# Kernel tuning notes

Measured on AMD Instinct MI355X. Metric: run time of the kernel, lower is better.

## Reference

```python
import jax, jax.numpy as jnp
import numpy as np

N, E, G = 20000, 240000, 64
F, H1, PE = 768, 128, 32
D = H1 + PE          # 160, GATv2 per-head dim
HEADS = 5
HC = HEADS * D       # 800
H2, OUT = 128, 16
NEG_SLOPE = 0.2


def setup_inputs() -> dict:
    key = jax.random.key(0)
    ks = jax.random.split(key, 24)
    s = 0.02
    inp = {
        'x': jax.random.normal(ks[0], (N, F), jnp.float32),
        'pe_enc': jax.random.normal(ks[1], (N, PE), jnp.float32),
        'edge_index': jax.random.randint(ks[2], (2, E), 0, N),
        'batch': jnp.sort(jax.random.randint(ks[3], (N,), 0, G)),
        'flat_weight': jax.random.uniform(ks[4], (N, 1), jnp.float32),
        'num_graphs': G,
        # params
        'W_pre': jax.random.normal(ks[5], (F, H1)) * s,
        'b_pre': jnp.zeros((H1,)),
        'W_l': jax.random.normal(ks[6], (D, HC)) * s,
        'b_l': jnp.zeros((HC,)),
        'W_r': jax.random.normal(ks[7], (D, HC)) * s,
        'b_r': jnp.zeros((HC,)),
        'att': jax.random.normal(ks[8], (HEADS, D)) * s,
        'gat_bias': jnp.zeros((HC,)),
        'W_gcn': jax.random.normal(ks[9], (HC, HC)) * s,
        'b_gcn': jnp.zeros((HC,)),
        'W_fc': jax.random.normal(ks[10], (2 * HC, H2)) * s,
        'b_fc': jnp.zeros((H2,)),
        'W_out': jax.random.normal(ks[11], (H2, OUT)) * s,
        'b_out': jnp.zeros((OUT,)),
    }
    return inp


def _forward(x, pe_enc, flat_weight, W_pre, b_pre, W_l, b_l, W_r, b_r, att,
             gat_bias, W_gcn, b_gcn, W_fc, b_fc, W_out, b_out,
             edge_index, batch, num_graphs):
    n = x.shape[0]
    # pre-FC + PE concat -> [N, D]
    h = jnp.concatenate([jax.nn.relu(x @ W_pre + b_pre), pe_enc], axis=1)
    # add self loops (PyG default for GATv2Conv and GCNConv)
    ar = jnp.arange(n)
    src = jnp.concatenate([edge_index[0], ar])
    dst = jnp.concatenate([edge_index[1], ar])
    # ---- GATv2Conv ----
    x_l = (h @ W_l + b_l).reshape(n, HEADS, D)
    x_r = (h @ W_r + b_r).reshape(n, HEADS, D)
    m = x_l[src] + x_r[dst]                                # [Et, H, D]
    score = (jnp.where(m > 0, m, NEG_SLOPE * m) * att).sum(-1)  # [Et, H]
    smax = jax.ops.segment_max(score, dst, num_segments=n)[dst]
    ex = jnp.exp(score - smax)
    den = jax.ops.segment_sum(ex, dst, num_segments=n)[dst]
    alpha = ex / den                                       # softmax per target
    agg = jax.ops.segment_sum(x_l[src] * alpha[..., None], dst, num_segments=n)
    g1 = jax.nn.relu(agg.reshape(n, HC) + gat_bias)
    # ---- GCNConv with symmetric normalization ----
    deg = jax.ops.segment_sum(jnp.ones_like(dst, dtype=g1.dtype), dst, num_segments=n)
    dinv = jnp.where(deg > 0, deg ** -0.5, 0.0)
    norm = dinv[src] * dinv[dst]
    hg = g1 @ W_gcn
    g2 = jax.nn.relu(jax.ops.segment_sum(hg[src] * norm[:, None], dst, num_segments=n) + b_gcn)
    # ---- weighted mean pool + max pool ----
    ps = jax.ops.segment_sum(g2 * flat_weight, batch, num_segments=num_graphs)
    ws = jnp.clip(jax.ops.segment_sum(flat_weight, batch, num_segments=num_graphs), 1e-6, None)
    pooled_mean = ps / ws
    mx = jax.ops.segment_max(g2, batch, num_segments=num_graphs)
    mx = jnp.where(jnp.isneginf(mx), 0.0, mx)  # empty graphs; g2 >= 0 after relu
    gfeat = jnp.concatenate([pooled_mean, mx], axis=1)     # [G, 2*HC]
    out = jax.nn.relu(gfeat @ W_fc + b_fc)                 # dropout is identity in eval
    return jax.nn.relu(out @ W_out + b_out)


def reference(x, pe_enc, edge_index, batch, flat_weight, num_graphs,
              W_pre, b_pre, W_l, b_l, W_r, b_r, att, gat_bias,
              W_gcn, b_gcn, W_fc, b_fc, W_out, b_out):
    return _forward(x, pe_enc, flat_weight, W_pre, b_pre, W_l, b_l, W_r, b_r,
                    att, gat_bias, W_gcn, b_gcn, W_fc, b_fc, W_out, b_out,
                    edge_index, batch, num_graphs)
```

## Files before the change

### kernel.cpp

```cpp
#include <hip/hip_runtime.h>
#include <hip/hip_bf16.h>

#define Nn     20000
#define Ee     240000
#define Gg     64
#define Ff     768
#define H1c    128
#define PEc    32
#define Dd     160
#define HEADSc 5
#define HCc    800
#define H2c    128
#define OUTc   16
#define ETot   (Ee + Nn)
#define NEG_SLOPE_F 0.2f

typedef short bf16x8 __attribute__((ext_vector_type(8)));
typedef float f32x4 __attribute__((ext_vector_type(4)));
typedef unsigned int u32;

__device__ __forceinline__ unsigned short bf_hi_rn(float v) {
    unsigned int u = __float_as_uint(v);
    return (unsigned short)((u + 0x7FFFu + ((u >> 16) & 1u)) >> 16);
}
__device__ __forceinline__ void bsplit(float v, unsigned short& h, unsigned short& l) {
    unsigned short hh = bf_hi_rn(v);
    float hf = __uint_as_float(((unsigned int)hh) << 16);
    l = bf_hi_rn(v - hf);
    h = hh;
}

__device__ __forceinline__ void gl_lds16(const unsigned short* g, unsigned short* l) {
    __builtin_amdgcn_global_load_lds(
        (const __attribute__((address_space(1))) u32*)g,
        (__attribute__((address_space(3))) u32*)l, 16, 0, 0);
}

__global__ void asplit_kernel(const float* __restrict__ A, unsigned short* __restrict__ Ah,
                              unsigned short* __restrict__ Al, int total4) {
    int i = blockIdx.x * 256 + threadIdx.x;
    if (i < total4) {
        float4 v = ((const float4*)A)[i];
        ushort4 h4, l4;
        bsplit(v.x, h4.x, l4.x);
        bsplit(v.y, h4.y, l4.y);
        bsplit(v.z, h4.z, l4.z);
        bsplit(v.w, h4.w, l4.w);
        ((ushort4*)Ah)[i] = h4;
        ((ushort4*)Al)[i] = l4;
    }
}

__global__ void wsplit_kernel(const float* __restrict__ W, unsigned short* __restrict__ Wh,
                              unsigned short* __restrict__ Wl, int K, int N) {
    int i = blockIdx.x * 256 + threadIdx.x;
    if (i < K * N) {
        int k = i / N, n = i % N;
        unsigned short h, l;
        bsplit(W[i], h, l);
        Wh[(size_t)n * K + k] = h;
        Wl[(size_t)n * K + k] = l;
    }
}

#define KCHUNK 32

template<int ROWS>
__device__ __forceinline__ void stage_tile(const unsigned short* __restrict__ gsrc, int ld,
                                           int row0, int maxRow, int k0,
                                           unsigned short* lbuf, int wave, int lane) {
    #pragma unroll
    for (int p = 0; p < ROWS / 64; ++p) {
        int rb = wave * 16 + p * 64;
        int r = rb + (lane >> 2);
        int gr = min(row0 + r, maxRow);
        const unsigned short* g = gsrc + (size_t)gr * ld + k0 + (lane & 3) * 8;
        gl_lds16(g, lbuf + rb * 32);
    }
}

template<int BM, int BN, int OUT_MODE>
__global__ __launch_bounds__(256)
void gemm3_kernel(const unsigned short* __restrict__ Ah, const unsigned short* __restrict__ Al,
                  const unsigned short* __restrict__ Bh, const unsigned short* __restrict__ Bl,
                  const float* __restrict__ bias, float* __restrict__ C,
                  unsigned short* __restrict__ Ch, unsigned short* __restrict__ Cl,
                  int M, int N, int K, int lda, int ldc, int relu) {
    constexpr int TM = BM / 32;
    constexpr int TN = BN / 32;
    __shared__ __attribute__((aligned(16))) unsigned short As_h[BM * 32];
    __shared__ __attribute__((aligned(16))) unsigned short As_l[BM * 32];
    __shared__ __attribute__((aligned(16))) unsigned short Bs_h[BN * 32];
    __shared__ __attribute__((aligned(16))) unsigned short Bs_l[BN * 32];

    int tid = threadIdx.x;
    int m0 = blockIdx.x * BM, n0 = blockIdx.y * BN;
    int wave = tid >> 6, lane = tid & 63;
    int wm = (wave >> 1) * (16 * TM);
    int wn = (wave & 1) * (16 * TN);
    int fr = lane & 15;
    int fq = (lane >> 4) * 8;

    f32x4 acc[TM][TN] = {};

    for (int k0 = 0; k0 < K; k0 += KCHUNK) {
        stage_tile<BM>(Ah, lda, m0, M - 1, k0, As_h, wave, lane);
        stage_tile<BM>(Al, lda, m0, M - 1, k0, As_l, wave, lane);
        stage_tile<BN>(Bh, K,   n0, N - 1, k0, Bs_h, wave, lane);
        stage_tile<BN>(Bl, K,   n0, N - 1, k0, Bs_l, wave, lane);
        __syncthreads();

        bf16x8 a_h[TM], a_l[TM], b_h[TN], b_l[TN];
        #pragma unroll
        for (int i = 0; i < TM; ++i) {
            a_h[i] = *(const bf16x8*)&As_h[(wm + i * 16 + fr) * 32 + fq];
            a_l[i] = *(const bf16x8*)&As_l[(wm + i * 16 + fr) * 32 + fq];
        }
        #pragma unroll
        for (int j = 0; j < TN; ++j) {
            b_h[j] = *(const bf16x8*)&Bs_h[(wn + j * 16 + fr) * 32 + fq];
            b_l[j] = *(const bf16x8*)&Bs_l[(wn + j * 16 + fr) * 32 + fq];
        }
        #pragma unroll
        for (int j = 0; j < TN; ++j) {
            #pragma unroll
            for (int i = 0; i < TM; ++i) {
                acc[i][j] = __builtin_amdgcn_mfma_f32_16x16x32_bf16(a_h[i], b_h[j], acc[i][j], 0, 0, 0);
                acc[i][j] = __builtin_amdgcn_mfma_f32_16x16x32_bf16(a_h[i], b_l[j], acc[i][j], 0, 0, 0);
                acc[i][j] = __builtin_amdgcn_mfma_f32_16x16x32_bf16(a_l[i], b_h[j], acc[i][j], 0, 0, 0);
            }
        }
        __syncthreads();
    }

    int cr = (lane >> 4) * 4, cc = lane & 15;
    #pragma unroll
    for (int i = 0; i < TM; ++i) {
        #pragma unroll
        for (int j = 0; j < TN; ++j) {
            int c = n0 + wn + j * 16 + cc;
            if (c >= N) continue;
            float bv = bias ? bias[c] : 0.f;
            #pragma unroll
            for (int reg = 0; reg < 4; ++reg) {
                int r = m0 + wm + i * 16 + cr + reg;
                if (r >= M) continue;
                float v = acc[i][j][reg] + bv;
                if (relu) v = fmaxf(v, 0.f);
                if (OUT_MODE == 0) {
                    C[(size_t)r * ldc + c] = v;
                } else {
                    unsigned short hh, ll;
                    bsplit(v, hh, ll);
                    Ch[(size_t)r * ldc + c] = hh;
                    Cl[(size_t)r * ldc + c] = ll;
                }
            }
        }
    }
}

__global__ void pe_copy_kernel(const float* __restrict__ pe, unsigned short* __restrict__ hh,
                               unsigned short* __restrict__ hl) {
    int i = blockIdx.x * 256 + threadIdx.x;
    if (i < Nn * PEc) {
        int n = i / PEc, j = i % PEc;
        unsigned short h, l;
        bsplit(pe[i], h, l);
        hh[(size_t)n * Dd + H1c + j] = h;
        hl[(size_t)n * Dd + H1c + j] = l;
    }
}

__global__ void count_kernel(const int* __restrict__ eidx, int* __restrict__ cnt) {
    int e = blockIdx.x * 256 + threadIdx.x;
    if (e < Ee) atomicAdd(&cnt[eidx[Ee + e]], 1);
}

#define NBLK 79
__global__ void scan1_kernel(const int* __restrict__ cnt, int* __restrict__ off,
                             int* __restrict__ bsum) {
    __shared__ int sh[256];
    int t = threadIdx.x, i = blockIdx.x * 256 + t;
    int v = (i < Nn) ? (cnt[i] + 1) : 0;
    sh[t] = v;
    __syncthreads();
    for (int ofs = 1; ofs < 256; ofs <<= 1) {
        int add = (t >= ofs) ? sh[t - ofs] : 0;
        __syncthreads();
        sh[t] += add;
        __syncthreads();
    }
    if (i < Nn) off[i] = sh[t] - v;
    if (t == 255) bsum[blockIdx.x] = sh[255];
}
__global__ void scan2_kernel(int* __restrict__ bsum) {
    if (threadIdx.x == 0) {
        int acc = 0;
        for (int b = 0; b < NBLK; ++b) { int v = bsum[b]; bsum[b] = acc; acc += v; }
    }
}
__global__ void scan3_kernel(const int* __restrict__ cnt, int* __restrict__ off,
                             int* __restrict__ nxt, float* __restrict__ dinv,
                             const int* __restrict__ bsum) {
    int i = blockIdx.x * 256 + threadIdx.x;
    if (i < Nn) {
        int o = off[i] + bsum[blockIdx.x];
        off[i] = o;
        nxt[i] = o;
        dinv[i] = rsqrtf((float)(cnt[i] + 1));
    }
    if (i == 0) off[Nn] = ETot;
}

__global__ void scatter_kernel(const int* __restrict__ eidx, int* __restrict__ nxt,
                               int* __restrict__ elist, int* __restrict__ edst) {
    int e = blockIdx.x * 256 + threadIdx.x;
    if (e < ETot) {
        int s, d;
        if (e < Ee) { s = eidx[e]; d = eidx[Ee + e]; }
        else        { s = e - Ee; d = s; }
        int slot = atomicAdd(&nxt[d], 1);
        elist[slot] = s;
        edst[slot] = d;
    }
}

#define FCH 8
__global__ __launch_bounds__(256)
void fused_gat_kernel(const float* __restrict__ xl, const float* __restrict__ xr,
                      const float* __restrict__ att, const int* __restrict__ elist,
                      const int* __restrict__ off, const float* __restrict__ gat_bias,
                      unsigned short* __restrict__ g1h, unsigned short* __restrict__ g1l) {
    int d = blockIdx.x;
    int t = threadIdx.x;
    __shared__ float sh_red[FCH][200];
    __shared__ float sh_sc[FCH][HEADSc];
    __shared__ float sh_w[FCH][HEADSc];
    __shared__ float sh_scale[HEADSc], sh_m[HEADSc], sh_den[HEADSc];
    __shared__ int sh_src[FCH];
    int e0 = off[d], e1 = off[d + 1];
    int cnt = e1 - e0;
    bool act = t < 200;
    int hd = act ? (t / 40) : 0;
    float4 vr = {0.f, 0.f, 0.f, 0.f}, va = {0.f, 0.f, 0.f, 0.f};
    if (act) {
        vr = ((const float4*)(xr + (size_t)d * HCc))[t];
        va = ((const float4*)att)[t];
    }
    if (t < HEADSc) { sh_m[t] = -1e30f; sh_den[t] = 0.f; }
    float4 acc = {0.f, 0.f, 0.f, 0.f};

    for (int base = 0; base < cnt; base += FCH) {
        int nc = min(FCH, cnt - base);
        if (t < FCH) sh_src[t] = elist[e0 + base + min(t, nc - 1)];
        __syncthreads();
        float4 vl[FCH];
        if (act) {
            #pragma unroll
            for (int e = 0; e < FCH; ++e)
                vl[e] = ((const float4*)(xl + (size_t)sh_src[e] * HCc))[t];
            #pragma unroll
            for (int e = 0; e < FCH; ++e) {
                float p = 0.f, m, lm;
                m = vl[e].x + vr.x; lm = fmaxf(m, 0.2f * m); p = fmaf(lm, va.x, p);
                m = vl[e].y + vr.y; lm = fmaxf(m, 0.2f * m); p = fmaf(lm, va.y, p);
                m = vl[e].z + vr.z; lm = fmaxf(m, 0.2f * m); p = fmaf(lm, va.z, p);
                m = vl[e].w + vr.w; lm = fmaxf(m, 0.2f * m); p = fmaf(lm, va.w, p);
                sh_red[e][t] = p;
            }
        }
        __syncthreads();
        if (t < 40) {
            int e = t & 7, h = t >> 3;
            float s = 0.f;
            const float* pr = &sh_red[e][h * 40];
            #pragma unroll
            for (int k = 0; k < 40; ++k) s += pr[k];
            sh_sc[e][h] = (e < nc) ? s : -1e30f;
        }
        if (t < HEADSc) {
            float mo = sh_m[t];
            float mn = mo;
            #pragma unroll
            for (int e = 0; e < FCH; ++e) mn = fmaxf(mn, sh_sc[e][t]);
            float sc = __expf(mo - mn);
            float den = sh_den[t] * sc;
            #pragma unroll
            for (int e = 0; e < FCH; ++e) {
                float w = __expf(sh_sc[e][t] - mn);
                sh_w[e][t] = w;
                den += w;
            }
            sh_den[t] = den;
            sh_m[t] = mn;
            sh_scale[t] = sc;
        }
        __syncthreads();
        if (act) {
            float sc = sh_scale[hd];
            acc.x *= sc; acc.y *= sc; acc.z *= sc; acc.w *= sc;
            #pragma unroll
            for (int e = 0; e < FCH; ++e) {
                float w = sh_w[e][hd];
                acc.x = fmaf(w, vl[e].x, acc.x);
                acc.y = fmaf(w, vl[e].y, acc.y);
                acc.z = fmaf(w, vl[e].z, acc.z);
                acc.w = fmaf(w, vl[e].w, acc.w);
            }
        }
    }
    if (act) {
        float inv = 1.f / sh_den[hd];
        float4 bv = ((const float4*)gat_bias)[t];
        ushort4 oh, ol;
        float v;
        v = fmaxf(fmaf(acc.x, inv, bv.x), 0.f); bsplit(v, oh.x, ol.x);
        v = fmaxf(fmaf(acc.y, inv, bv.y), 0.f); bsplit(v, oh.y, ol.y);
        v = fmaxf(fmaf(acc.z, inv, bv.z), 0.f); bsplit(v, oh.z, ol.z);
        v = fmaxf(fmaf(acc.w, inv, bv.w), 0.f); bsplit(v, oh.w, ol.w);
        *(ushort4*)(g1h + (size_t)d * HCc + 4 * t) = oh;
        *(ushort4*)(g1l + (size_t)d * HCc + 4 * t) = ol;
    }
}

__global__ __launch_bounds__(256)
void gcn_kernel(const float* __restrict__ hg, const float* __restrict__ dinv,
                const int* __restrict__ elist, const int* __restrict__ off,
                const float* __restrict__ b_gcn, float* __restrict__ g2) {
    int d = blockIdx.x;
    int t = threadIdx.x;
    __shared__ int src_s[64];
    __shared__ float w_s[64];
    int e0 = off[d], e1 = off[d + 1];
    int cnt = e1 - e0;
    float di = dinv[d];
    float4 acc = {0.f, 0.f, 0.f, 0.f};
    for (int base = 0; base < cnt; base += 64) {
        int nc = min(64, cnt - base);
        if (t < nc) {
            int s = elist[e0 + base + t];
            src_s[t] = s;
            w_s[t] = dinv[s];
        }
        __syncthreads();
        if (t < 200) {
            for (int el = 0; el < nc; ++el) {
                const float4* p = (const float4*)(hg + (size_t)src_s[el] * HCc);
                float w = w_s[el];
                float4 v = p[t];
                acc.x = fmaf(w, v.x, acc.x);
                acc.y = fmaf(w, v.y, acc.y);
                acc.z = fmaf(w, v.z, acc.z);
                acc.w = fmaf(w, v.w, acc.w);
            }
        }
        __syncthreads();
    }
    if (t < 200) {
        float4 bv = ((const float4*)b_gcn)[t];
        float4 o;
        o.x = fmaxf(acc.x * di + bv.x, 0.f);
        o.y = fmaxf(acc.y * di + bv.y, 0.f);
        o.z = fmaxf(acc.z * di + bv.z, 0.f);
        o.w = fmaxf(acc.w * di + bv.w, 0.f);
        *(float4*)(g2 + (size_t)d * HCc + 4 * t) = o;
    }
}

__global__ void bounds_kernel(const int* __restrict__ batch, int* __restrict__ starts) {
    int g = threadIdx.x;
    if (g <= Gg) {
        if (g == Gg) { starts[Gg] = Nn; return; }
        int lo = 0, hi = Nn;
        while (lo < hi) {
            int mid = (lo + hi) >> 1;
            if (batch[mid] < g) lo = mid + 1; else hi = mid;
        }
        starts[g] = lo;
    }
}

#define PSL 4
__global__ __launch_bounds__(256)
void pool1_kernel(const float* __restrict__ g2, const float* __restrict__ fw,
                  const int* __restrict__ starts, float* __restrict__ pw,
                  float* __restrict__ pmean, float* __restrict__ pmax) {
    int g = blockIdx.x, s = blockIdx.y, t = threadIdx.x;
    int n0 = starts[g], n1 = starts[g + 1];
    int len = n1 - n0;
    int q0 = n0 + (int)(((long long)len * s) / PSL);
    int q1 = n0 + (int)(((long long)len * (s + 1)) / PSL);
    __shared__ float red[256];
    float wsum = 0.f;
    for (int n = q0 + t; n < q1; n += 256) wsum += fw[n];
    red[t] = wsum;
    __syncthreads();
    for (int ofs = 128; ofs > 0; ofs >>= 1) {
        if (t < ofs) red[t] += red[t + ofs];
        __syncthreads();
    }
    if (t == 0) pw[g * PSL + s] = red[0];
    if (t < 200) {
        float4 sum = {0.f, 0.f, 0.f, 0.f};
        float4 mx = {0.f, 0.f, 0.f, 0.f};
        for (int n = q0; n < q1; ++n) {
            float w = fw[n];
            float4 v = ((const float4*)(g2 + (size_t)n * HCc))[t];
            sum.x = fmaf(w, v.x, sum.x); sum.y = fmaf(w, v.y, sum.y);
            sum.z = fmaf(w, v.z, sum.z); sum.w = fmaf(w, v.w, sum.w);
            mx.x = fmaxf(mx.x, v.x); mx.y = fmaxf(mx.y, v.y);
            mx.z = fmaxf(mx.z, v.z); mx.w = fmaxf(mx.w, v.w);
        }
        size_t o = ((size_t)g * PSL + s) * HCc + 4 * t;
        *(float4*)(pmean + o) = sum;
        *(float4*)(pmax + o) = mx;
    }
}
__global__ __launch_bounds__(256)
void pool2_kernel(const float* __restrict__ pw, const float* __restrict__ pmean,
                  const float* __restrict__ pmax, float* __restrict__ gfeat) {
    int g = blockIdx.x, t = threadIdx.x;
    if (t >= 200) return;
    float wsg = 0.f;
    #pragma unroll
    for (int s = 0; s < PSL; ++s) wsg += pw[g * PSL + s];
    wsg = fmaxf(wsg, 1e-6f);
    float inv = 1.f / wsg;
    float4 sum = {0.f, 0.f, 0.f, 0.f};
    float4 mx = {0.f, 0.f, 0.f, 0.f};
    #pragma unroll
    for (int s = 0; s < PSL; ++s) {
        size_t o = ((size_t)g * PSL + s) * HCc + 4 * t;
        float4 a = *(const float4*)(pmean + o);
        float4 b = *(const float4*)(pmax + o);
        sum.x += a.x; sum.y += a.y; sum.z += a.z; sum.w += a.w;
        mx.x = fmaxf(mx.x, b.x); mx.y = fmaxf(mx.y, b.y);
        mx.z = fmaxf(mx.z, b.z); mx.w = fmaxf(mx.w, b.w);
    }
    float* gm = gfeat + (size_t)g * (2 * HCc);
    sum.x *= inv; sum.y *= inv; sum.z *= inv; sum.w *= inv;
    *(float4*)(gm + 4 * t) = sum;
    *(float4*)(gm + HCc + 4 * t) = mx;
}

__global__ __launch_bounds__(128)
void head_kernel(const float* __restrict__ gfeat, const float* __restrict__ W_fc,
                 const float* __restrict__ b_fc, const float* __restrict__ W_out,
                 const float* __restrict__ b_out, float* __restrict__ out) {
    int g = blockIdx.x;
    int t = threadIdx.x;
    __shared__ float gf[2 * HCc];
    __shared__ float fc1[H2c];
    for (int i = t; i < 2 * HCc; i += 128) gf[i] = gfeat[(size_t)g * (2 * HCc) + i];
    __syncthreads();
    float a0 = 0.f, a1 = 0.f, a2 = 0.f, a3 = 0.f;
    for (int k = 0; k < 2 * HCc; k += 4) {
        a0 = fmaf(gf[k],     W_fc[(size_t)k * H2c + t], a0);
        a1 = fmaf(gf[k + 1], W_fc[(size_t)(k + 1) * H2c + t], a1);
        a2 = fmaf(gf[k + 2], W_fc[(size_t)(k + 2) * H2c + t], a2);
        a3 = fmaf(gf[k + 3], W_fc[(size_t)(k + 3) * H2c + t], a3);
    }
    fc1[t] = fmaxf(b_fc[t] + ((a0 + a1) + (a2 + a3)), 0.f);
    __syncthreads();
    if (t < OUTc) {
        float o = b_out[t];
        #pragma unroll 8
        for (int k = 0; k < H2c; ++k) o += fc1[k] * W_out[k * OUTc + t];
        out[g * OUTc + t] = fmaxf(o, 0.f);
    }
}

extern "C" void kernel_launch(void* const* d_in, const int* in_sizes, int n_in,
                              void* d_out, int out_size, void* d_ws, size_t ws_size,
                              hipStream_t stream) {
    (void)in_sizes; (void)n_in; (void)out_size; (void)ws_size;
    const float* x        = (const float*)d_in[0];
    const float* pe       = (const float*)d_in[1];
    const int*   eidx     = (const int*)d_in[2];
    const int*   batch    = (const int*)d_in[3];
    const float* fw       = (const float*)d_in[4];
    const float* W_pre    = (const float*)d_in[6];
    const float* b_pre    = (const float*)d_in[7];
    const float* W_l      = (const float*)d_in[8];
    const float* b_l      = (const float*)d_in[9];
    const float* W_r      = (const float*)d_in[10];
    const float* b_r      = (const float*)d_in[11];
    const float* att      = (const float*)d_in[12];
    const float* gat_bias = (const float*)d_in[13];
    const float* W_gcn    = (const float*)d_in[14];
    const float* b_gcn    = (const float*)d_in[15];
    const float* W_fc     = (const float*)d_in[16];
    const float* b_fc     = (const float*)d_in[17];
    const float* W_out    = (const float*)d_in[18];
    const float* b_out    = (const float*)d_in[19];
    float* out = (float*)d_out;

    char* p = (char*)d_ws;
    auto alloc = [&](size_t bytes) {
        char* r = p;
        p += (bytes + 255) & ~(size_t)255;
        return r;
    };
    unsigned short* hh = (unsigned short*)alloc((size_t)Nn * Dd * 2 * 2);
    unsigned short* hl = hh + (size_t)Nn * Dd;
    float* bufA = (float*)alloc((size_t)Nn * HCc * 4);
    float* bufB = (float*)alloc((size_t)Nn * HCc * 4);
    float* bufC = (float*)alloc((size_t)Nn * HCc * 4);
    int*   cnt    = (int*)alloc((size_t)Nn * 4);
    int*   off    = (int*)alloc((size_t)(Nn + 1) * 4);
    int*   nxt    = (int*)alloc((size_t)Nn * 4);
    float* dinv   = (float*)alloc((size_t)Nn * 4);
    int*   elist  = (int*)alloc((size_t)ETot * 4);
    int*   edst   = (int*)alloc((size_t)ETot * 4);
    int*   starts = (int*)alloc((size_t)(Gg + 1) * 4);
    float* gfeat  = (float*)alloc((size_t)Gg * 2 * HCc * 4);
    int*   bsum   = (int*)alloc((size_t)NBLK * 4);
    float* pw     = (float*)alloc((size_t)Gg * PSL * 4);
    float* pmean  = (float*)alloc((size_t)Gg * PSL * HCc * 4);
    float* pmax   = (float*)alloc((size_t)Gg * PSL * HCc * 4);
    unsigned short* WpreTh = (unsigned short*)alloc((size_t)Ff * H1c * 2 * 2);
    unsigned short* WpreTl = WpreTh + (size_t)Ff * H1c;
    unsigned short* WlTh   = (unsigned short*)alloc((size_t)Dd * HCc * 2 * 2);
    unsigned short* WlTl   = WlTh + (size_t)Dd * HCc;
    unsigned short* WrTh   = (unsigned short*)alloc((size_t)Dd * HCc * 2 * 2);
    unsigned short* WrTl   = WrTh + (size_t)Dd * HCc;
    unsigned short* WgTh   = (unsigned short*)alloc((size_t)HCc * HCc * 2 * 2);
    unsigned short* WgTl   = WgTh + (size_t)HCc * HCc;

    unsigned short* xh  = (unsigned short*)bufC;
    unsigned short* xlo = xh + (size_t)Nn * Ff;
    unsigned short* g1h = (unsigned short*)bufC;
    unsigned short* g1l = g1h + (size_t)Nn * HCc;

    hipMemsetAsync(cnt, 0, (size_t)Nn * 4, stream);
    count_kernel<<<(Ee + 255) / 256, 256, 0, stream>>>(eidx, cnt);
    scan1_kernel<<<NBLK, 256, 0, stream>>>(cnt, off, bsum);
    scan2_kernel<<<1, 64, 0, stream>>>(bsum);
    scan3_kernel<<<NBLK, 256, 0, stream>>>(cnt, off, nxt, dinv, bsum);
    scatter_kernel<<<(ETot + 255) / 256, 256, 0, stream>>>(eidx, nxt, elist, edst);

    asplit_kernel<<<(Nn * Ff / 4 + 255) / 256, 256, 0, stream>>>(x, xh, xlo, Nn * Ff / 4);
    wsplit_kernel<<<(Ff * H1c + 255) / 256, 256, 0, stream>>>(W_pre, WpreTh, WpreTl, Ff, H1c);
    wsplit_kernel<<<(Dd * HCc + 255) / 256, 256, 0, stream>>>(W_l, WlTh, WlTl, Dd, HCc);
    wsplit_kernel<<<(Dd * HCc + 255) / 256, 256, 0, stream>>>(W_r, WrTh, WrTl, Dd, HCc);
    wsplit_kernel<<<(HCc * HCc + 255) / 256, 256, 0, stream>>>(W_gcn, WgTh, WgTl, HCc, HCc);

    {
        dim3 grid((Nn + 63) / 64, (H1c + 63) / 64);
        gemm3_kernel<64, 64, 1><<<grid, 256, 0, stream>>>(
            xh, xlo, WpreTh, WpreTl, b_pre, nullptr, hh, hl,
            Nn, H1c, Ff, Ff, Dd, 1);
    }
    pe_copy_kernel<<<(Nn * PEc + 255) / 256, 256, 0, stream>>>(pe, hh, hl);

    {
        dim3 grid((Nn + 127) / 128, (HCc + 127) / 128);
        gemm3_kernel<128, 128, 0><<<grid, 256, 0, stream>>>(
            hh, hl, WlTh, WlTl, b_l, bufA, nullptr, nullptr,
            Nn, HCc, Dd, Dd, HCc, 0);
        gemm3_kernel<128, 128, 0><<<grid, 256, 0, stream>>>(
            hh, hl, WrTh, WrTl, b_r, bufB, nullptr, nullptr,
            Nn, HCc, Dd, Dd, HCc, 0);
    }

    fused_gat_kernel<<<Nn, 256, 0, stream>>>(bufA, bufB, att, elist, off,
                                             gat_bias, g1h, g1l);

    {
        dim3 grid((Nn + 127) / 128, (HCc + 127) / 128);
        gemm3_kernel<128, 128, 0><<<grid, 256, 0, stream>>>(
            g1h, g1l, WgTh, WgTl, nullptr, bufA, nullptr, nullptr,
            Nn, HCc, HCc, HCc, HCc, 0);
    }
    gcn_kernel<<<Nn, 256, 0, stream>>>(bufA, dinv, elist, off, b_gcn, bufB);

    bounds_kernel<<<1, 128, 0, stream>>>(batch, starts);
    {
        dim3 pg(Gg, PSL);
        pool1_kernel<<<pg, 256, 0, stream>>>(bufB, fw, starts, pw, pmean, pmax);
    }
    pool2_kernel<<<Gg, 256, 0, stream>>>(pw, pmean, pmax, gfeat);
    head_kernel<<<Gg, 128, 0, stream>>>(gfeat, W_fc, b_fc, W_out, b_out, out);
}
```

Measured before the change: 805.0 us.

## Merge left/right GAT projections into one GEMM and batch edge gathers

```diff
diff --git a/kernel.cpp b/kernel.cpp
--- a/kernel.cpp
+++ b/kernel.cpp
@@ -83,7 +83,8 @@
 __global__ __launch_bounds__(256)
 void gemm3_kernel(const unsigned short* __restrict__ Ah, const unsigned short* __restrict__ Al,
                   const unsigned short* __restrict__ Bh, const unsigned short* __restrict__ Bl,
-                  const float* __restrict__ bias, float* __restrict__ C,
+                  const float* __restrict__ bias, const float* __restrict__ bias2,
+                  float* __restrict__ C, float* __restrict__ C2,
                   unsigned short* __restrict__ Ch, unsigned short* __restrict__ Cl,
                   int M, int N, int K, int lda, int ldc, int relu) {
     constexpr int TM = BM / 32;
@@ -140,7 +141,9 @@
         for (int j = 0; j < TN; ++j) {
             int c = n0 + wn + j * 16 + cc;
             if (c >= N) continue;
-            float bv = bias ? bias[c] : 0.f;
+            float bv;
+            if (OUT_MODE == 2) bv = (c < HCc) ? bias[c] : bias2[c - HCc];
+            else bv = bias ? bias[c] : 0.f;
             #pragma unroll
             for (int reg = 0; reg < 4; ++reg) {
                 int r = m0 + wm + i * 16 + cr + reg;
@@ -149,6 +152,9 @@
                 if (relu) v = fmaxf(v, 0.f);
                 if (OUT_MODE == 0) {
                     C[(size_t)r * ldc + c] = v;
+                } else if (OUT_MODE == 2) {
+                    if (c < HCc) C[(size_t)r * HCc + c] = v;
+                    else         C2[(size_t)r * HCc + (c - HCc)] = v;
                 } else {
                     unsigned short hh, ll;
                     bsplit(v, hh, ll);
@@ -214,7 +220,7 @@
 }
 
 __global__ void scatter_kernel(const int* __restrict__ eidx, int* __restrict__ nxt,
-                               int* __restrict__ elist, int* __restrict__ edst) {
+                               int* __restrict__ elist) {
     int e = blockIdx.x * 256 + threadIdx.x;
     if (e < ETot) {
         int s, d;
@@ -222,11 +228,10 @@
         else        { s = e - Ee; d = s; }
         int slot = atomicAdd(&nxt[d], 1);
         elist[slot] = s;
-        edst[slot] = d;
-    }
-}
-
-#define FCH 8
+    }
+}
+
+#define FCH 16
 __global__ __launch_bounds__(256)
 void fused_gat_kernel(const float* __restrict__ xl, const float* __restrict__ xr,
                       const float* __restrict__ att, const int* __restrict__ elist,
@@ -273,11 +278,13 @@
         __syncthreads();
         if (t < 40) {
             int e = t & 7, h = t >> 3;
-            float s = 0.f;
-            const float* pr = &sh_red[e][h * 40];
-            #pragma unroll
-            for (int k = 0; k < 40; ++k) s += pr[k];
-            sh_sc[e][h] = (e < nc) ? s : -1e30f;
+            float s0 = 0.f, s1 = 0.f;
+            const float* p0 = &sh_red[e][h * 40];
+            const float* p1 = &sh_red[e + 8][h * 40];
+            #pragma unroll
+            for (int k = 0; k < 40; ++k) { s0 += p0[k]; s1 += p1[k]; }
+            sh_sc[e][h]     = (e < nc)     ? s0 : -1e30f;
+            sh_sc[e + 8][h] = (e + 8 < nc) ? s1 : -1e30f;
         }
         if (t < HEADSc) {
             float mo = sh_m[t];
@@ -324,40 +331,45 @@
     }
 }
 
+#define GCH 16
 __global__ __launch_bounds__(256)
 void gcn_kernel(const float* __restrict__ hg, const float* __restrict__ dinv,
                 const int* __restrict__ elist, const int* __restrict__ off,
                 const float* __restrict__ b_gcn, float* __restrict__ g2) {
     int d = blockIdx.x;
     int t = threadIdx.x;
-    __shared__ int src_s[64];
-    __shared__ float w_s[64];
+    __shared__ int src_s[GCH];
+    __shared__ float w_s[GCH];
     int e0 = off[d], e1 = off[d + 1];
     int cnt = e1 - e0;
     float di = dinv[d];
+    bool act = t < 200;
     float4 acc = {0.f, 0.f, 0.f, 0.f};
-    for (int base = 0; base < cnt; base += 64) {
-        int nc = min(64, cnt - base);
-        if (t < nc) {
-            int s = elist[e0 + base + t];
+    for (int base = 0; base < cnt; base += GCH) {
+        int nc = min(GCH, cnt - base);
+        if (t < GCH) {
+            int s = elist[e0 + base + min(t, nc - 1)];
             src_s[t] = s;
-            w_s[t] = dinv[s];
-        }
-        __syncthreads();
-        if (t < 200) {
-            for (int el = 0; el < nc; ++el) {
-                const float4* p = (const float4*)(hg + (size_t)src_s[el] * HCc);
-                float w = w_s[el];
-                float4 v = p[t];
-                acc.x = fmaf(w, v.x, acc.x);
-                acc.y = fmaf(w, v.y, acc.y);
-                acc.z = fmaf(w, v.z, acc.z);
-                acc.w = fmaf(w, v.w, acc.w);
+            w_s[t] = (t < nc) ? dinv[s] : 0.f;
+        }
+        __syncthreads();
+        if (act) {
+            float4 vl[GCH];
+            #pragma unroll
+            for (int e = 0; e < GCH; ++e)
+                vl[e] = ((const float4*)(hg + (size_t)src_s[e] * HCc))[t];
+            #pragma unroll
+            for (int e = 0; e < GCH; ++e) {
+                float w = w_s[e];
+                acc.x = fmaf(w, vl[e].x, acc.x);
+                acc.y = fmaf(w, vl[e].y, acc.y);
+                acc.z = fmaf(w, vl[e].z, acc.z);
+                acc.w = fmaf(w, vl[e].w, acc.w);
             }
         }
         __syncthreads();
     }
-    if (t < 200) {
+    if (act) {
         float4 bv = ((const float4*)b_gcn)[t];
         float4 o;
         o.x = fmaxf(acc.x * di + bv.x, 0.f);
@@ -512,7 +524,6 @@
     int*   nxt    = (int*)alloc((size_t)Nn * 4);
     float* dinv   = (float*)alloc((size_t)Nn * 4);
     int*   elist  = (int*)alloc((size_t)ETot * 4);
-    int*   edst   = (int*)alloc((size_t)ETot * 4);
     int*   starts = (int*)alloc((size_t)(Gg + 1) * 4);
     float* gfeat  = (float*)alloc((size_t)Gg * 2 * HCc * 4);
     int*   bsum   = (int*)alloc((size_t)NBLK * 4);
@@ -521,10 +532,8 @@
     float* pmax   = (float*)alloc((size_t)Gg * PSL * HCc * 4);
     unsigned short* WpreTh = (unsigned short*)alloc((size_t)Ff * H1c * 2 * 2);
     unsigned short* WpreTl = WpreTh + (size_t)Ff * H1c;
-    unsigned short* WlTh   = (unsigned short*)alloc((size_t)Dd * HCc * 2 * 2);
-    unsigned short* WlTl   = WlTh + (size_t)Dd * HCc;
-    unsigned short* WrTh   = (unsigned short*)alloc((size_t)Dd * HCc * 2 * 2);
-    unsigned short* WrTl   = WrTh + (size_t)Dd * HCc;
+    unsigned short* WlrTh  = (unsigned short*)alloc((size_t)Dd * 2 * HCc * 2 * 2);
+    unsigned short* WlrTl  = WlrTh + (size_t)Dd * 2 * HCc;
     unsigned short* WgTh   = (unsigned short*)alloc((size_t)HCc * HCc * 2 * 2);
     unsigned short* WgTl   = WgTh + (size_t)HCc * HCc;
 
@@ -538,39 +547,37 @@
     scan1_kernel<<<NBLK, 256, 0, stream>>>(cnt, off, bsum);
     scan2_kernel<<<1, 64, 0, stream>>>(bsum);
     scan3_kernel<<<NBLK, 256, 0, stream>>>(cnt, off, nxt, dinv, bsum);
-    scatter_kernel<<<(ETot + 255) / 256, 256, 0, stream>>>(eidx, nxt, elist, edst);
+    scatter_kernel<<<(ETot + 255) / 256, 256, 0, stream>>>(eidx, nxt, elist);
 
     asplit_kernel<<<(Nn * Ff / 4 + 255) / 256, 256, 0, stream>>>(x, xh, xlo, Nn * Ff / 4);
     wsplit_kernel<<<(Ff * H1c + 255) / 256, 256, 0, stream>>>(W_pre, WpreTh, WpreTl, Ff, H1c);
-    wsplit_kernel<<<(Dd * HCc + 255) / 256, 256, 0, stream>>>(W_l, WlTh, WlTl, Dd, HCc);
-    wsplit_kernel<<<(Dd * HCc + 255) / 256, 256, 0, stream>>>(W_r, WrTh, WrTl, Dd, HCc);
+    wsplit_kernel<<<(Dd * HCc + 255) / 256, 256, 0, stream>>>(W_l, WlrTh, WlrTl, Dd, HCc);
+    wsplit_kernel<<<(Dd * HCc + 255) / 256, 256, 0, stream>>>(
+        W_r, WlrTh + (size_t)HCc * Dd, WlrTl + (size_t)HCc * Dd, Dd, HCc);
     wsplit_kernel<<<(HCc * HCc + 255) / 256, 256, 0, stream>>>(W_gcn, WgTh, WgTl, HCc, HCc);
 
     {
         dim3 grid((Nn + 63) / 64, (H1c + 63) / 64);
         gemm3_kernel<64, 64, 1><<<grid, 256, 0, stream>>>(
-            xh, xlo, WpreTh, WpreTl, b_pre, nullptr, hh, hl,
+            xh, xlo, WpreTh, WpreTl, b_pre, nullptr, nullptr, nullptr, hh, hl,
             Nn, H1c, Ff, Ff, Dd, 1);
     }
     pe_copy_kernel<<<(Nn * PEc + 255) / 256, 256, 0, stream>>>(pe, hh, hl);
+
+    {
+        dim3 grid((Nn + 127) / 128, (2 * HCc + 127) / 128);
+        gemm3_kernel<128, 128, 2><<<grid, 256, 0, stream>>>(
+            hh, hl, WlrTh, WlrTl, b_l, b_r, bufA, bufB, nullptr, nullptr,
+            Nn, 2 * HCc, Dd, Dd, HCc, 0);
+    }
+
+    fused_gat_kernel<<<Nn, 256, 0, stream>>>(bufA, bufB, att, elist, off,
+                                             gat_bias, g1h, g1l);
 
     {
         dim3 grid((Nn + 127) / 128, (HCc + 127) / 128);
         gemm3_kernel<128, 128, 0><<<grid, 256, 0, stream>>>(
-            hh, hl, WlTh, WlTl, b_l, bufA, nullptr, nullptr,
-            Nn, HCc, Dd, Dd, HCc, 0);
-        gemm3_kernel<128, 128, 0><<<grid, 256, 0, stream>>>(
-            hh, hl, WrTh, WrTl, b_r, bufB, nullptr, nullptr,
-            Nn, HCc, Dd, Dd, HCc, 0);
-    }
-
-    fused_gat_kernel<<<Nn, 256, 0, stream>>>(bufA, bufB, att, elist, off,
-                                             gat_bias, g1h, g1l);
-
-    {
-        dim3 grid((Nn + 127) / 128, (HCc + 127) / 128);
-        gemm3_kernel<128, 128, 0><<<grid, 256, 0, stream>>>(
-            g1h, g1l, WgTh, WgTl, nullptr, bufA, nullptr, nullptr,
+            g1h, g1l, WgTh, WgTl, nullptr, nullptr, bufA, nullptr, nullptr, nullptr,
             Nn, HCc, HCc, HCc, HCc, 0);
     }
     gcn_kernel<<<Nn, 256, 0, stream>>>(bufA, dinv, elist, off, b_gcn, bufB);
```

Result: no change. 795.4 us (-1.2%).
